# Optimization experiments

Hardware: AMD Instinct MI355X
Metric: run time of the kernel (lower is better)

Reference implementation:

```python
import jax, jax.numpy as jnp
import numpy as np

NUM_GROUPS = 32
EPS = 1e-5
HEADS = 8
DIM_HEAD = 64


def group_norm(x, w, b):
    # x: [B, C, L]; normalize over (C/G, L) per group
    B, C, L = x.shape
    xg = x.reshape(B, NUM_GROUPS, C // NUM_GROUPS, L)
    mu = jnp.mean(xg, axis=(2, 3), keepdims=True)
    var = jnp.var(xg, axis=(2, 3), keepdims=True)
    xn = ((xg - mu) * jax.lax.rsqrt(var + EPS)).reshape(B, C, L)
    return xn * w[None, :, None] + b[None, :, None]


def setup_inputs() -> dict:
    key = jax.random.key(0)
    k1, k2, k3 = jax.random.split(key, 3)
    dim, hidden = 512, HEADS * DIM_HEAD
    B, L = 4, 2048
    x = jax.random.normal(k1, (B, dim, L), dtype=jnp.float32)
    gn_w = jnp.ones((dim,), jnp.float32)
    gn_b = jnp.zeros((dim,), jnp.float32)
    w_qkv = jax.random.normal(k2, (3 * hidden, dim), jnp.float32) * (dim ** -0.5)
    w_out = jax.random.normal(k3, (dim, hidden), jnp.float32) * (hidden ** -0.5)
    b_out = jnp.zeros((dim,), jnp.float32)
    return {"x": x, "gn_w": gn_w, "gn_b": gn_b, "w_qkv": w_qkv, "w_out": w_out, "b_out": b_out}


def reference(x, gn_w, gn_b, w_qkv, w_out, b_out):
    B, C, L = x.shape
    scale = DIM_HEAD ** -0.5
    nx = group_norm(x, gn_w, gn_b)
    # 1x1 conv == channel matmul: [3H*D, C] x [B, C, L] -> [B, 3H*D, L]
    qkv = jnp.einsum('oc,bcl->bol', w_qkv, nx)
    q, k, v = jnp.split(qkv, 3, axis=1)
    rs = lambda t: t.reshape(B, HEADS, DIM_HEAD, L)
    q, k, v = rs(q) * scale, rs(k), rs(v)
    sim = jnp.einsum('bhdi,bhdj->bhij', q, k)         # [B,H,L,L]
    attn = jax.nn.softmax(sim, axis=-1)
    out = jnp.einsum('bhij,bhdj->bhdi', attn, v)       # [B,H,D,L]
    out = out.reshape(B, HEADS * DIM_HEAD, L)
    proj = jnp.einsum('oc,bcl->bol', w_out, out) + b_out[None, :, None]
    return proj + x
```

## Files before the change

### kernel.cpp

```cpp
#include <hip/hip_runtime.h>

#define DEVI __device__ __forceinline__

typedef unsigned short u16;
typedef unsigned int u32;
typedef __attribute__((ext_vector_type(8))) __bf16 bf16x8;
typedef __attribute__((ext_vector_type(2))) __bf16 bf16x2;
typedef __attribute__((ext_vector_type(4))) float f32x4;
typedef __attribute__((ext_vector_type(16))) float f32x16;
typedef __attribute__((ext_vector_type(4))) u32 u32x4;

DEVI u16 f2bf(float f){
  u32 u = __float_as_uint(f);
  return (u16)((u + 0x7FFFu + ((u >> 16) & 1u)) >> 16);
}
DEVI u32 pk2(float lo, float hi){
  bf16x2 t; t[0] = (__bf16)lo; t[1] = (__bf16)hi;
  return __builtin_bit_cast(u32, t);
}

__global__ __launch_bounds__(256) void pre_kernel(const float* __restrict__ x,
                                                  float2* __restrict__ pstat,
                                                  const float* __restrict__ wq,
                                                  const float* __restrict__ wo,
                                                  u16* __restrict__ wqb,
                                                  u16* __restrict__ wob){
  int bid = blockIdx.x, tid = threadIdx.x;
  if (bid < 512){
    int bg = bid >> 2, qt = bid & 3;
    const float4* xin = (const float4*)(x + (size_t)bg*32768 + qt*8192);
    float s1 = 0.f, s2 = 0.f;
    #pragma unroll
    for (int i = 0; i < 8; ++i){
      float4 v = xin[tid + i*256];
      s1 += v.x + v.y + v.z + v.w;
      s2 += v.x*v.x + v.y*v.y + v.z*v.z + v.w*v.w;
    }
    __shared__ float red[8];
    int lane = tid & 63, w = tid >> 6;
    for (int off = 32; off; off >>= 1){
      s1 += __shfl_down(s1, off);
      s2 += __shfl_down(s2, off);
    }
    if (lane == 0){ red[w] = s1; red[4 + w] = s2; }
    __syncthreads();
    if (tid == 0){
      pstat[bid] = make_float2(red[0]+red[1]+red[2]+red[3],
                               red[4]+red[5]+red[6]+red[7]);
    }
  } else {
    int t = (bid - 512) * 256 + tid;
    const int NQ4 = (1536*512)/4;
    float4 v; u16* dst;
    if (t < NQ4){ v = ((const float4*)wq)[t]; dst = wqb + t*4; }
    else        { int u_ = t - NQ4; v = ((const float4*)wo)[u_]; dst = wob + u_*4; }
    ushort4 s;
    s.x = f2bf(v.x); s.y = f2bf(v.y); s.z = f2bf(v.z); s.w = f2bf(v.w);
    *(ushort4*)dst = s;
  }
}

__global__ __launch_bounds__(256) void normtrans_kernel(const float* __restrict__ x,
                                                        const float2* __restrict__ pstat,
                                                        const float* __restrict__ gw,
                                                        const float* __restrict__ gb,
                                                        u16* __restrict__ nxT){
  int b = blockIdx.z, c0 = blockIdx.y * 64, l0 = blockIdx.x * 64;
  __shared__ u16 T[64][72];
  int tid = threadIdx.x;
  #pragma unroll
  for (int rep = 0; rep < 2; ++rep){
    int task = tid + rep*256;
    int r = task >> 3, cc = task & 7;
    int ch = c0 + r;
    int bg = b*32 + (ch >> 4);
    float s1 = 0.f, s2 = 0.f;
    #pragma unroll
    for (int i = 0; i < 4; ++i){
      float2 p = pstat[bg*4 + i];
      s1 += p.x; s2 += p.y;
    }
    float mu = s1 * (1.f/32768.f);
    float rsg = rsqrtf(s2 * (1.f/32768.f) - mu*mu + 1e-5f);
    float ga = gw[ch] * rsg;
    float be = gb[ch] - mu * ga;
    const float4* src = (const float4*)(x + ((size_t)(b*512 + ch))*2048 + l0 + cc*8);
    float4 v0 = src[0], v1 = src[1];
    ushort4 o0, o1;
    o0.x = f2bf(v0.x*ga + be); o0.y = f2bf(v0.y*ga + be);
    o0.z = f2bf(v0.z*ga + be); o0.w = f2bf(v0.w*ga + be);
    o1.x = f2bf(v1.x*ga + be); o1.y = f2bf(v1.y*ga + be);
    o1.z = f2bf(v1.z*ga + be); o1.w = f2bf(v1.w*ga + be);
    *(ushort4*)&T[r][cc*8]     = o0;
    *(ushort4*)&T[r][cc*8 + 4] = o1;
  }
  __syncthreads();
  #pragma unroll
  for (int rep = 0; rep < 2; ++rep){
    int task = tid + rep*256;
    int r = task >> 3, cc = task & 7;
    u16 tmp[8];
    #pragma unroll
    for (int i = 0; i < 8; ++i) tmp[i] = T[cc*8 + i][r];
    *(uint4*)(nxT + ((size_t)(b*2048 + l0 + r))*512 + c0 + cc*8) = *(uint4*)tmp;
  }
}

template<int MODE>
__global__ __launch_bounds__(256) void gemm_kernel(const u16* __restrict__ A,
                                                   const u16* __restrict__ Bm,
                                                   u16* __restrict__ q_o,
                                                   u16* __restrict__ k_o,
                                                   u16* __restrict__ v_o,
                                                   const float* __restrict__ bo,
                                                   const float* __restrict__ xres,
                                                   float* __restrict__ out){
  int b  = blockIdx.z;
  int n0 = blockIdx.x * 128, m0 = blockIdx.y * 128;
  int tid = threadIdx.x, w = tid >> 6, lane = tid & 63, lq = lane >> 4, lr = lane & 15;
  int wm = (w >> 1) * 64, wn = (w & 1) * 64;
  __shared__ u16 Al[2][128][40], Bl[2][128][40];
  f32x4 acc[4][4] = {};
  const u16* Bb = Bm + (size_t)b * 2048 * 512;

  for (int k0 = 0; k0 < 512; k0 += 64){
    #pragma unroll
    for (int rep = 0; rep < 4; ++rep){
      int task = tid + rep*256;
      int row = task >> 3, kc = task & 7;
      *(uint4*)&Al[kc>>2][row][(kc&3)*8] = *(const uint4*)(A  + (size_t)(m0+row)*512 + k0 + kc*8);
      *(uint4*)&Bl[kc>>2][row][(kc&3)*8] = *(const uint4*)(Bb + (size_t)(n0+row)*512 + k0 + kc*8);
    }
    __syncthreads();
    #pragma unroll
    for (int half = 0; half < 2; ++half){
      bf16x8 af[4], bfr[4];
      #pragma unroll
      for (int i = 0; i < 4; ++i) af[i]  = *(const bf16x8*)&Al[half][wm + i*16 + lr][lq*8];
      #pragma unroll
      for (int j = 0; j < 4; ++j) bfr[j] = *(const bf16x8*)&Bl[half][wn + j*16 + lr][lq*8];
      #pragma unroll
      for (int i = 0; i < 4; ++i)
        #pragma unroll
        for (int j = 0; j < 4; ++j)
          acc[i][j] = __builtin_amdgcn_mfma_f32_16x16x32_bf16(af[i], bfr[j], acc[i][j], 0, 0, 0);
    }
    __syncthreads();
  }

  if (MODE == 0){
    const float QSCALE = 0.125f * 1.4426950408889634f;
    #pragma unroll
    for (int i = 0; i < 4; ++i){
      int o0  = m0 + wm + i*16 + lq*4;
      int cls = o0 >> 9;
      int hh  = (o0 >> 6) & 7;
      int d0  = o0 & 63;
      size_t hbase = (size_t)(b*8+hh) * 2048 * 64;
      #pragma unroll
      for (int j = 0; j < 4; ++j){
        int l = n0 + wn + j*16 + lr;
        f32x4 v = acc[i][j];
        if (cls == 0){
          ushort4 s;
          s.x = f2bf(v[0]*QSCALE); s.y = f2bf(v[1]*QSCALE);
          s.z = f2bf(v[2]*QSCALE); s.w = f2bf(v[3]*QSCALE);
          *(ushort4*)(q_o + hbase + (size_t)l*64 + d0) = s;
        } else if (cls == 1){
          size_t off = (size_t)(((l>>5)*4 + (d0>>4)))*512
                     + ((d0>>3)&1)*256 + (l&31)*8 + (d0&7);
          ushort4 s;
          s.x = f2bf(v[0]); s.y = f2bf(v[1]); s.z = f2bf(v[2]); s.w = f2bf(v[3]);
          *(ushort4*)(k_o + hbase + off) = s;
        } else {
          size_t off = (size_t)(((l>>4)*2 + (d0>>5)))*512
                     + ((l>>3)&1)*256 + (l&7);
          #pragma unroll
          for (int r = 0; r < 4; ++r)
            v_o[hbase + off + ((d0+r)&31)*8] = f2bf(v[r]);
        }
      }
    }
  } else {
    #pragma unroll
    for (int i = 0; i < 4; ++i){
      int o0 = m0 + wm + i*16 + lq*4;
      #pragma unroll
      for (int j = 0; j < 4; ++j){
        int l = n0 + wn + j*16 + lr;
        #pragma unroll
        for (int r = 0; r < 4; ++r){
          int o = o0 + r;
          size_t idx = ((size_t)b*512 + o)*2048 + l;
          out[idx] = acc[i][j][r] + bo[o] + xres[idx];
        }
      }
    }
  }
}

__global__ __launch_bounds__(256, 2) void attn_kernel(const u16* __restrict__ qT,
                                                      const u16* __restrict__ kF,
                                                      const u16* __restrict__ vF,
                                                      u16* __restrict__ ao){
  int flat = blockIdx.x;
  int xcd = flat & 7, tt = flat >> 3;
  int bh = xcd*4 + (tt & 3);
  int qb = tt >> 2;
  int tid = threadIdx.x, w = tid >> 6, l = tid & 63;
  int l31 = l & 31, h = l >> 5;
  int q0 = qb*128 + w*32;
  size_t hoff = (size_t)bh * 2048 * 64;

  const u16* qp = qT + hoff + (size_t)(q0 + l31)*64 + 8*h;
  bf16x8 qf0 = *(const bf16x8*)(qp);
  bf16x8 qf1 = *(const bf16x8*)(qp + 16);
  bf16x8 qf2 = *(const bf16x8*)(qp + 32);
  bf16x8 qf3 = *(const bf16x8*)(qp + 48);

  const u16* kbase = kF + hoff + (size_t)l*8;
  const u16* vbase = vF + hoff + (size_t)l*8;

  f32x16 o0 = {}, o1 = {};
  float m = -1e30f, lsum = 0.f;

  bf16x8 kA0,kA1,kA2,kA3, kB0,kB1,kB2,kB3;
  bf16x8 vA0,vA1,vA2,vA3, vB0,vB1,vB2,vB3;
  f32x16 sA, sB;
  bf16x8 Bf0, Bf1;

#define LDK(P, t) { const u16* kt_ = kbase + (t)*2048;                         \
    P##0 = *(const bf16x8*)(kt_);        P##1 = *(const bf16x8*)(kt_ + 512);   \
    P##2 = *(const bf16x8*)(kt_ + 1024); P##3 = *(const bf16x8*)(kt_ + 1536); }
#define LDV(P, t) { const u16* vt_ = vbase + (t)*2048;                         \
    P##0 = *(const bf16x8*)(vt_);        P##1 = *(const bf16x8*)(vt_ + 512);   \
    P##2 = *(const bf16x8*)(vt_ + 1024); P##3 = *(const bf16x8*)(vt_ + 1536); }
#define QKT(S, P) {                                                            \
    S = (f32x16){};                                                            \
    __builtin_amdgcn_s_setprio(1);                                             \
    S = __builtin_amdgcn_mfma_f32_32x32x16_bf16(P##0, qf0, S, 0, 0, 0);        \
    S = __builtin_amdgcn_mfma_f32_32x32x16_bf16(P##1, qf1, S, 0, 0, 0);        \
    S = __builtin_amdgcn_mfma_f32_32x32x16_bf16(P##2, qf2, S, 0, 0, 0);        \
    S = __builtin_amdgcn_mfma_f32_32x32x16_bf16(P##3, qf3, S, 0, 0, 0);        \
    __builtin_amdgcn_s_setprio(0); }
#define SMAX(S) { \
    float c0 = fmaxf(S[0],S[1]),  c1 = fmaxf(S[2],S[3]);                       \
    float c2 = fmaxf(S[4],S[5]),  c3 = fmaxf(S[6],S[7]);                       \
    float c4 = fmaxf(S[8],S[9]),  c5 = fmaxf(S[10],S[11]);                     \
    float c6 = fmaxf(S[12],S[13]),c7 = fmaxf(S[14],S[15]);                     \
    c0 = fmaxf(c0,c1); c2 = fmaxf(c2,c3); c4 = fmaxf(c4,c5); c6 = fmaxf(c6,c7);\
    c0 = fmaxf(c0,c2); c4 = fmaxf(c4,c6); c0 = fmaxf(c0,c4);                   \
    c0 = fmaxf(c0, __shfl_xor(c0, 32));                                        \
    if (__any(c0 > m + 8.f)){                                                  \
      float nm = fmaxf(m, c0);                                                 \
      float alpha = __builtin_amdgcn_exp2f(m - nm);                            \
      m = nm; lsum *= alpha;                                                   \
      _Pragma("unroll")                                                        \
      for (int i = 0; i < 16; ++i){ o0[i] *= alpha; o1[i] *= alpha; }          \
    }                                                                          \
    float p[16];                                                               \
    _Pragma("unroll")                                                          \
    for (int i = 0; i < 16; ++i) p[i] = __builtin_amdgcn_exp2f(S[i] - m);      \
    float t0 = p[0]+p[1],  t1 = p[2]+p[3],  t2 = p[4]+p[5],  t3 = p[6]+p[7];   \
    float t4 = p[8]+p[9],  t5 = p[10]+p[11],t6 = p[12]+p[13],t7 = p[14]+p[15]; \
    t0 += t1; t2 += t3; t4 += t5; t6 += t7; t0 += t2; t4 += t6; t0 += t4;      \
    lsum += t0 + __shfl_xor(t0, 32);                                           \
    u32 a0 = pk2(p[0],p[1]),   a1 = pk2(p[2],p[3]);                            \
    u32 a2 = pk2(p[4],p[5]),   a3 = pk2(p[6],p[7]);                            \
    u32 a4 = pk2(p[8],p[9]),   a5 = pk2(p[10],p[11]);                          \
    u32 a6 = pk2(p[12],p[13]), a7 = pk2(p[14],p[15]);                          \
    u32 x0 = __shfl_xor((int)a0,32), x1 = __shfl_xor((int)a1,32);              \
    u32 x2 = __shfl_xor((int)a2,32), x3 = __shfl_xor((int)a3,32);              \
    u32 x4 = __shfl_xor((int)a4,32), x5 = __shfl_xor((int)a5,32);              \
    u32 x6 = __shfl_xor((int)a6,32), x7 = __shfl_xor((int)a7,32);              \
    u32x4 wb0, wb1;                                                            \
    wb0[0] = h ? x2 : a0;  wb0[1] = h ? x3 : a1;                               \
    wb0[2] = h ? a2 : x0;  wb0[3] = h ? a3 : x1;                               \
    wb1[0] = h ? x6 : a4;  wb1[1] = h ? x7 : a5;                               \
    wb1[2] = h ? a6 : x4;  wb1[3] = h ? a7 : x5;                               \
    Bf0 = __builtin_bit_cast(bf16x8, wb0);                                     \
    Bf1 = __builtin_bit_cast(bf16x8, wb1); }
#define PVA(P) {                                                               \
    __builtin_amdgcn_s_setprio(1);                                             \
    o0 = __builtin_amdgcn_mfma_f32_32x32x16_bf16(P##0, Bf0, o0, 0, 0, 0);      \
    o1 = __builtin_amdgcn_mfma_f32_32x32x16_bf16(P##1, Bf0, o1, 0, 0, 0);      \
    o0 = __builtin_amdgcn_mfma_f32_32x32x16_bf16(P##2, Bf1, o0, 0, 0, 0);      \
    o1 = __builtin_amdgcn_mfma_f32_32x32x16_bf16(P##3, Bf1, o1, 0, 0, 0);      \
    __builtin_amdgcn_s_setprio(0); }

  LDK(kA, 0);
  QKT(sA, kA);
  LDK(kB, 1);
  LDV(vA, 0);
  LDV(vB, 1);

  for (int t = 0; t < 64; t += 2){
    int t2 = (t+2 < 64) ? t+2 : 63;
    int t3 = (t+3 < 64) ? t+3 : 63;
    QKT(sB, kB);
    LDK(kA, t2);
    SMAX(sA);
    PVA(vA);
    LDV(vA, t2);
    QKT(sA, kA);
    LDK(kB, t3);
    SMAX(sB);
    PVA(vB);
    LDV(vB, t3);
  }

#undef LDK
#undef LDV
#undef QKT
#undef SMAX
#undef PVA

  float inv = 1.f / lsum;
  int b_ = bh >> 3, hh = bh & 7;
  size_t obase = ((size_t)(b_*2048) + q0 + l31)*512 + hh*64 + 4*h;
  #pragma unroll
  for (int s4 = 0; s4 < 4; ++s4){
    ushort4 st;
    st.x = f2bf(o0[s4*4+0]*inv); st.y = f2bf(o0[s4*4+1]*inv);
    st.z = f2bf(o0[s4*4+2]*inv); st.w = f2bf(o0[s4*4+3]*inv);
    *(ushort4*)(ao + obase + s4*8) = st;
  }
  #pragma unroll
  for (int s4 = 0; s4 < 4; ++s4){
    ushort4 st;
    st.x = f2bf(o1[s4*4+0]*inv); st.y = f2bf(o1[s4*4+1]*inv);
    st.z = f2bf(o1[s4*4+2]*inv); st.w = f2bf(o1[s4*4+3]*inv);
    *(ushort4*)(ao + obase + 32 + s4*8) = st;
  }
}

extern "C" void kernel_launch(void* const* d_in, const int* in_sizes, int n_in,
                              void* d_out, int out_size, void* d_ws, size_t ws_size,
                              hipStream_t stream) {
  const float* x    = (const float*)d_in[0];
  const float* gw   = (const float*)d_in[1];
  const float* gb   = (const float*)d_in[2];
  const float* wqkv = (const float*)d_in[3];
  const float* wout = (const float*)d_in[4];
  const float* bout = (const float*)d_in[5];
  float* out = (float*)d_out;
  char* ws = (char*)d_ws;

  const size_t MB8 = (size_t)4*512*2048*2;
  u16* ao  = (u16*)(ws);
  u16* nxT = (u16*)(ws + MB8);
  u16* wqb = (u16*)(ws + 2*MB8);
  u16* wob = (u16*)(ws + 2*MB8 + 1572864);
  u16* qT  = (u16*)(ws + 2*MB8 + 2097152);
  u16* kF  = qT + (size_t)4*8*2048*64;
  u16* vF  = kF + (size_t)4*8*2048*64;
  float2* pstat = (float2*)qT;

  pre_kernel<<<1536, 256, 0, stream>>>(x, pstat, wqkv, wout, wqb, wob);
  normtrans_kernel<<<dim3(32, 8, 4), 256, 0, stream>>>(x, pstat, gw, gb, nxT);
  gemm_kernel<0><<<dim3(16, 12, 4), 256, 0, stream>>>(wqb, nxT, qT, kF, vF,
                                                      nullptr, nullptr, nullptr);
  attn_kernel<<<512, 256, 0, stream>>>(qT, kF, vF, ao);
  gemm_kernel<1><<<dim3(16, 4, 4), 256, 0, stream>>>(wob, ao, nullptr, nullptr, nullptr,
                                                     bout, x, out);
}
```

Measured before the change: 173.1 us.

## Stage QKV GEMM epilogue through LDS for coalesced stores; peel attention loop tail

The QKV projection epilogue now writes converted bf16 tiles into shared memory (reusing the GEMM staging buffer) and then emits fully coalesced 16-byte global stores in the q, k-fragment and v-fragment layouts. This replaces scattered ushort4 and scalar 2-byte stores, notably for V. The attention loop switches to pointer increments and peels the final iteration, which removes the clamped redundant loads past the end. It also reshapes the max-reduction tree. The cost is an extra LDS round trip and a barrier in the epilogue, plus possible bank conflicts on the transposed LDS writes.

```diff
diff --git a/kernel.cpp b/kernel.cpp
--- a/kernel.cpp
+++ b/kernel.cpp
@@ -119,7 +119,9 @@
   int n0 = blockIdx.x * 128, m0 = blockIdx.y * 128;
   int tid = threadIdx.x, w = tid >> 6, lane = tid & 63, lq = lane >> 4, lr = lane & 15;
   int wm = (w >> 1) * 64, wn = (w & 1) * 64;
-  __shared__ u16 Al[2][128][40], Bl[2][128][40];
+  __shared__ u16 lds[20480];
+  u16 (*Al)[128][40] = (u16(*)[128][40])(lds);
+  u16 (*Bl)[128][40] = (u16(*)[128][40])(lds + 10240);
   f32x4 acc[4][4] = {};
   const u16* Bb = Bm + (size_t)b * 2048 * 512;
 
@@ -150,36 +152,58 @@
 
   if (MODE == 0){
     const float QSCALE = 0.125f * 1.4426950408889634f;
-    #pragma unroll
-    for (int i = 0; i < 4; ++i){
-      int o0  = m0 + wm + i*16 + lq*4;
-      int cls = o0 >> 9;
-      int hh  = (o0 >> 6) & 7;
-      int d0  = o0 & 63;
-      size_t hbase = (size_t)(b*8+hh) * 2048 * 64;
-      #pragma unroll
-      for (int j = 0; j < 4; ++j){
-        int l = n0 + wn + j*16 + lr;
-        f32x4 v = acc[i][j];
-        if (cls == 0){
-          ushort4 s;
-          s.x = f2bf(v[0]*QSCALE); s.y = f2bf(v[1]*QSCALE);
-          s.z = f2bf(v[2]*QSCALE); s.w = f2bf(v[3]*QSCALE);
-          *(ushort4*)(q_o + hbase + (size_t)l*64 + d0) = s;
-        } else if (cls == 1){
-          size_t off = (size_t)(((l>>5)*4 + (d0>>4)))*512
-                     + ((d0>>3)&1)*256 + (l&31)*8 + (d0&7);
-          ushort4 s;
-          s.x = f2bf(v[0]); s.y = f2bf(v[1]); s.z = f2bf(v[2]); s.w = f2bf(v[3]);
-          *(ushort4*)(k_o + hbase + off) = s;
-        } else {
-          size_t off = (size_t)(((l>>4)*2 + (d0>>5)))*512
-                     + ((l>>3)&1)*256 + (l&7);
+    int cls = m0 >> 9;
+    float scale = (cls == 0) ? QSCALE : 1.f;
+    if (cls < 2){
+      #pragma unroll
+      for (int i = 0; i < 4; ++i){
+        int o_local = wm + i*16 + lq*4;
+        #pragma unroll
+        for (int j = 0; j < 4; ++j){
+          int ll = wn + j*16 + lr;
+          ushort4 s4v;
+          s4v.x = f2bf(acc[i][j][0]*scale); s4v.y = f2bf(acc[i][j][1]*scale);
+          s4v.z = f2bf(acc[i][j][2]*scale); s4v.w = f2bf(acc[i][j][3]*scale);
+          *(ushort4*)&lds[ll*136 + o_local] = s4v;
+        }
+      }
+    } else {
+      #pragma unroll
+      for (int i = 0; i < 4; ++i){
+        int o_local = wm + i*16 + lq*4;
+        #pragma unroll
+        for (int j = 0; j < 4; ++j){
+          int ll = wn + j*16 + lr;
           #pragma unroll
           for (int r = 0; r < 4; ++r)
-            v_o[hbase + off + ((d0+r)&31)*8] = f2bf(v[r]);
+            lds[(o_local + r)*136 + ll] = f2bf(acc[i][j][r]);
         }
       }
+    }
+    __syncthreads();
+    int hh_base = (m0 >> 6) & 7;
+    #pragma unroll
+    for (int c = 0; c < 8; ++c){
+      int g = tid + c*256;
+      int h_loc = g >> 10, r = g & 1023;
+      size_t hbase = (size_t)(b*8 + hh_base + h_loc) * 2048 * 64;
+      uint4 data; u16* gdst;
+      if (cls == 0){
+        int l_loc = (g >> 3) & 127, dc = g & 7;
+        data = *(const uint4*)&lds[l_loc*136 + h_loc*64 + dc*8];
+        gdst = q_o + hbase + (size_t)(n0 + l_loc)*64 + dc*8;
+      } else if (cls == 1){
+        int l_in = r & 31, m1 = (r >> 5) & 1, vv = r >> 6;
+        int l_loc = (vv >> 2)*32 + l_in, dc = ((vv & 3) << 1) | m1;
+        data = *(const uint4*)&lds[l_loc*136 + h_loc*64 + dc*8];
+        gdst = k_o + hbase + (size_t)n0*64 + (size_t)r*8;
+      } else {
+        int d31 = r & 31, m1 = (r >> 5) & 1, w4 = r >> 6;
+        int d = (w4 & 1)*32 + d31, ll0 = (w4 >> 1)*16 + m1*8;
+        data = *(const uint4*)&lds[(h_loc*64 + d)*136 + ll0];
+        gdst = v_o + hbase + (size_t)n0*64 + (size_t)r*8;
+      }
+      *(uint4*)gdst = data;
     }
   } else {
     #pragma unroll
@@ -229,12 +253,9 @@
   f32x16 sA, sB;
   bf16x8 Bf0, Bf1;
 
-#define LDK(P, t) { const u16* kt_ = kbase + (t)*2048;                         \
-    P##0 = *(const bf16x8*)(kt_);        P##1 = *(const bf16x8*)(kt_ + 512);   \
-    P##2 = *(const bf16x8*)(kt_ + 1024); P##3 = *(const bf16x8*)(kt_ + 1536); }
-#define LDV(P, t) { const u16* vt_ = vbase + (t)*2048;                         \
-    P##0 = *(const bf16x8*)(vt_);        P##1 = *(const bf16x8*)(vt_ + 512);   \
-    P##2 = *(const bf16x8*)(vt_ + 1024); P##3 = *(const bf16x8*)(vt_ + 1536); }
+#define LDKP(P, ptr) {                                                         \
+    P##0 = *(const bf16x8*)(ptr);        P##1 = *(const bf16x8*)(ptr + 512);   \
+    P##2 = *(const bf16x8*)(ptr + 1024); P##3 = *(const bf16x8*)(ptr + 1536); }
 #define QKT(S, P) {                                                            \
     S = (f32x16){};                                                            \
     __builtin_amdgcn_s_setprio(1);                                             \
@@ -244,12 +265,14 @@
     S = __builtin_amdgcn_mfma_f32_32x32x16_bf16(P##3, qf3, S, 0, 0, 0);        \
     __builtin_amdgcn_s_setprio(0); }
 #define SMAX(S) { \
-    float c0 = fmaxf(S[0],S[1]),  c1 = fmaxf(S[2],S[3]);                       \
-    float c2 = fmaxf(S[4],S[5]),  c3 = fmaxf(S[6],S[7]);                       \
-    float c4 = fmaxf(S[8],S[9]),  c5 = fmaxf(S[10],S[11]);                     \
-    float c6 = fmaxf(S[12],S[13]),c7 = fmaxf(S[14],S[15]);                     \
-    c0 = fmaxf(c0,c1); c2 = fmaxf(c2,c3); c4 = fmaxf(c4,c5); c6 = fmaxf(c6,c7);\
-    c0 = fmaxf(c0,c2); c4 = fmaxf(c4,c6); c0 = fmaxf(c0,c4);                   \
+    float m0_ = fmaxf(fmaxf(S[0],S[1]),S[2]);                                  \
+    float m1_ = fmaxf(fmaxf(S[3],S[4]),S[5]);                                  \
+    float m2_ = fmaxf(fmaxf(S[6],S[7]),S[8]);                                  \
+    float m3_ = fmaxf(fmaxf(S[9],S[10]),S[11]);                                \
+    float m4_ = fmaxf(fmaxf(S[12],S[13]),S[14]);                               \
+    float n0_ = fmaxf(fmaxf(m0_,m1_),m2_);                                     \
+    float n1_ = fmaxf(fmaxf(m3_,m4_),S[15]);                                   \
+    float c0 = fmaxf(n0_, n1_);                                                \
     c0 = fmaxf(c0, __shfl_xor(c0, 32));                                        \
     if (__any(c0 > m + 8.f)){                                                  \
       float nm = fmaxf(m, c0);                                                 \
@@ -288,29 +311,36 @@
     o1 = __builtin_amdgcn_mfma_f32_32x32x16_bf16(P##3, Bf1, o1, 0, 0, 0);      \
     __builtin_amdgcn_s_setprio(0); }
 
-  LDK(kA, 0);
+  LDKP(kA, kbase);
   QKT(sA, kA);
-  LDK(kB, 1);
-  LDV(vA, 0);
-  LDV(vB, 1);
-
-  for (int t = 0; t < 64; t += 2){
-    int t2 = (t+2 < 64) ? t+2 : 63;
-    int t3 = (t+3 < 64) ? t+3 : 63;
+  { const u16* p1 = kbase + 2048; LDKP(kB, p1); }
+  LDKP(vA, vbase);
+  { const u16* p1 = vbase + 2048; LDKP(vB, p1); }
+
+  const u16* kpA = kbase + 4096;
+  const u16* kpB = kbase + 6144;
+  const u16* vpA = vbase + 4096;
+  const u16* vpB = vbase + 6144;
+
+  for (int it = 0; it < 31; ++it){
     QKT(sB, kB);
-    LDK(kA, t2);
+    LDKP(kA, kpA); kpA += 4096;
     SMAX(sA);
     PVA(vA);
-    LDV(vA, t2);
+    LDKP(vA, vpA); vpA += 4096;
     QKT(sA, kA);
-    LDK(kB, t3);
+    LDKP(kB, kpB); kpB += 4096;
     SMAX(sB);
     PVA(vB);
-    LDV(vB, t3);
-  }
-
-#undef LDK
-#undef LDV
+    LDKP(vB, vpB); vpB += 4096;
+  }
+  QKT(sB, kB);
+  SMAX(sA);
+  PVA(vA);
+  SMAX(sB);
+  PVA(vB);
+
+#undef LDKP
 #undef QKT
 #undef SMAX
 #undef PVA
```

New measurement: 175.2 us. Within noise of the previous version (+1.2%).
